# Optimization experiments

Hardware: AMD Instinct MI355X
Metric: run time of the kernel (lower is better)

Reference implementation:

```python
import jax, jax.numpy as jnp
import numpy as np

D_IN = 1024
D_OUT = 1024
NUM_HEAD = 16
HEAD_DIM = D_OUT // NUM_HEAD
CTX = 2048


def setup_inputs() -> dict:
    key = jax.random.key(0)
    ks = jax.random.split(key, 7)
    s = 0.02
    x = jax.random.normal(ks[0], (2, CTX, D_IN), dtype=jnp.float32)
    Wq = jax.random.normal(ks[1], (D_IN, D_OUT), dtype=jnp.float32) * s
    Wk = jax.random.normal(ks[2], (D_IN, D_OUT), dtype=jnp.float32) * s
    Wv = jax.random.normal(ks[3], (D_IN, D_OUT), dtype=jnp.float32) * s
    Wo = jax.random.normal(ks[4], (D_OUT, D_OUT), dtype=jnp.float32) * s
    bo = jax.random.normal(ks[5], (D_OUT,), dtype=jnp.float32) * s
    return {"x": x, "Wq": Wq, "Wk": Wk, "Wv": Wv, "Wo": Wo, "bo": bo}


def reference(x, Wq, Wk, Wv, Wo, bo):
    B, T, _ = x.shape
    # QKV projections, split into heads: [B, H, T, hd]
    def split_heads(y):
        return y.reshape(B, T, NUM_HEAD, HEAD_DIM).transpose(0, 2, 1, 3)
    q = split_heads(x @ Wq)
    k = split_heads(x @ Wk)
    v = split_heads(x @ Wv)
    # scaled causal attention scores [B, H, T, T]
    scores = jnp.einsum("bhqd,bhkd->bhqk", q, k) / jnp.sqrt(
        jnp.asarray(HEAD_DIM, dtype=x.dtype))
    causal = jnp.tril(jnp.ones((T, T), dtype=bool))  # mask buffer triu(diag=1) -> keep lower tri
    scores = jnp.where(causal[None, None], scores, jnp.asarray(-jnp.inf, dtype=x.dtype))
    attn = jax.nn.softmax(scores, axis=-1)
    # dropout with droprate=0.0 is identity
    ctx = jnp.einsum("bhqk,bhkd->bhqd", attn, v)
    ctx = ctx.transpose(0, 2, 1, 3).reshape(B, T, D_OUT)
    return ctx @ Wo + bo
```

## Files before the change

### kernel.cpp

```cpp
#include <hip/hip_runtime.h>

typedef __bf16 bf16x8 __attribute__((ext_vector_type(8)));
typedef float f32x4 __attribute__((ext_vector_type(4)));

__device__ inline float bf2f(unsigned short u) {
    unsigned int x = ((unsigned int)u) << 16;
    return __builtin_bit_cast(float, x);
}
__device__ inline unsigned short f2bf(float f) {
    unsigned int x = __builtin_bit_cast(unsigned int, f);
    x += 0x7fff + ((x >> 16) & 1);
    return (unsigned short)(x >> 16);
}

__device__ __forceinline__ void gl_lds16(const unsigned short* g, unsigned short* l)
{
    __builtin_amdgcn_global_load_lds(
        (const __attribute__((address_space(1))) void*)g,
        (__attribute__((address_space(3))) void*)l, 16, 0, 0);
}

__global__ __launch_bounds__(256)
void prep(const float* __restrict__ x, unsigned short* __restrict__ xb,
          const float* __restrict__ Wq, const float* __restrict__ Wk,
          const float* __restrict__ Wv, unsigned short* __restrict__ wT)
{
    __shared__ unsigned short T[64][72];
    if (blockIdx.x < 2048) {
        const size_t i = ((size_t)blockIdx.x * 256 + threadIdx.x) * 8;
        float4 a = *reinterpret_cast<const float4*>(x + i);
        float4 b = *reinterpret_cast<const float4*>(x + i + 4);
        unsigned short t[8] = { f2bf(a.x), f2bf(a.y), f2bf(a.z), f2bf(a.w),
                                f2bf(b.x), f2bf(b.y), f2bf(b.z), f2bf(b.w) };
        *reinterpret_cast<uint4*>(xb + i) = *reinterpret_cast<uint4*>(t);
        return;
    }
    const int blk = blockIdx.x - 2048;
    const int z = blk >> 8, within = blk & 255;
    const float* W = (z == 0) ? Wq : (z == 1) ? Wk : Wv;
    unsigned short* dstBase = wT + (size_t)z * 1024 * 1024;
    const int k0 = (within >> 4) * 64, n0 = (within & 15) * 64;
    const int r = threadIdx.x >> 2, c0 = (threadIdx.x & 3) * 16;
    const float* src = W + (size_t)(k0 + r) * 1024 + n0 + c0;
    #pragma unroll
    for (int j = 0; j < 16; j += 4) {
        float4 f = *reinterpret_cast<const float4*>(src + j);
        T[r][c0 + j]     = f2bf(f.x);
        T[r][c0 + j + 1] = f2bf(f.y);
        T[r][c0 + j + 2] = f2bf(f.z);
        T[r][c0 + j + 3] = f2bf(f.w);
    }
    __syncthreads();
    unsigned short* dst = dstBase + (size_t)(n0 + r) * 1024 + k0 + c0;
    #pragma unroll
    for (int h = 0; h < 2; ++h) {
        unsigned short t8[8];
        #pragma unroll
        for (int j = 0; j < 8; ++j) t8[j] = T[c0 + h * 8 + j][r];
        *reinterpret_cast<uint4*>(dst + h * 8) = *reinterpret_cast<uint4*>(t8);
    }
}

__global__ __launch_bounds__(256)
void wconv(const float* __restrict__ W, unsigned short* __restrict__ wT)
{
    __shared__ unsigned short T[64][72];
    const int k0 = blockIdx.y * 64, n0 = blockIdx.x * 64;
    const int r = threadIdx.x >> 2, c0 = (threadIdx.x & 3) * 16;
    const float* src = W + (size_t)(k0 + r) * 1024 + n0 + c0;
    #pragma unroll
    for (int j = 0; j < 16; j += 4) {
        float4 f = *reinterpret_cast<const float4*>(src + j);
        T[r][c0 + j]     = f2bf(f.x);
        T[r][c0 + j + 1] = f2bf(f.y);
        T[r][c0 + j + 2] = f2bf(f.z);
        T[r][c0 + j + 3] = f2bf(f.w);
    }
    __syncthreads();
    unsigned short* dst = wT + (size_t)(n0 + r) * 1024 + k0 + c0;
    #pragma unroll
    for (int h = 0; h < 2; ++h) {
        unsigned short t8[8];
        #pragma unroll
        for (int j = 0; j < 8; ++j) t8[j] = T[c0 + h * 8 + j][r];
        *reinterpret_cast<uint4*>(dst + h * 8) = *reinterpret_cast<uint4*>(t8);
    }
}

template <int MODE>
__global__ __launch_bounds__(256)
void gemm128(const unsigned short* __restrict__ A,
             const unsigned short* __restrict__ BT,
             void* __restrict__ C0, void* __restrict__ C1,
             void* __restrict__ C2, const float* __restrict__ bias)
{
    __shared__ unsigned short As[128 * 32];
    __shared__ unsigned short Bs[128 * 32];

    const int tid = threadIdx.x;
    const int wave = tid >> 6, lane = tid & 63, quad = lane >> 4, l16 = lane & 15;
    const int wm = wave >> 1, wn = wave & 1;
    const int mBase = blockIdx.y * 128, nBase = blockIdx.x * 128;

    f32x4 acc[4][4] = {};

    const int srow = lane >> 2, sko = (lane & 3) * 8;

    for (int kb = 0; kb < 1024; kb += 32) {
        __syncthreads();
        #pragma unroll
        for (int j = 0; j < 2; ++j) {
            const int seg = wave * 2 + j;
            gl_lds16(A  + (size_t)(mBase + seg * 16 + srow) * 1024 + kb + sko,
                     As + seg * 512);
            gl_lds16(BT + (size_t)(nBase + seg * 16 + srow) * 1024 + kb + sko,
                     Bs + seg * 512);
        }
        __syncthreads();

        bf16x8 af[4], bf[4];
        #pragma unroll
        for (int t = 0; t < 4; ++t) {
            af[t] = *reinterpret_cast<const bf16x8*>(&As[(wm * 64 + t * 16 + l16) * 32 + quad * 8]);
            bf[t] = *reinterpret_cast<const bf16x8*>(&Bs[(wn * 64 + t * 16 + l16) * 32 + quad * 8]);
        }
        #pragma unroll
        for (int ti = 0; ti < 4; ++ti)
            #pragma unroll
            for (int tj = 0; tj < 4; ++tj)
                acc[ti][tj] = __builtin_amdgcn_mfma_f32_16x16x32_bf16(
                    af[ti], bf[tj], acc[ti][tj], 0, 0, 0);
    }

    #pragma unroll
    for (int ti = 0; ti < 4; ++ti) {
        const int row0 = mBase + wm * 64 + ti * 16 + quad * 4;
        #pragma unroll
        for (int tj = 0; tj < 4; ++tj) {
            const int col = nBase + wn * 64 + tj * 16 + l16;
            if constexpr (MODE == 0) {
                if (col < 1024) {
                    unsigned short* qb = (unsigned short*)C0;
                    #pragma unroll
                    for (int i = 0; i < 4; ++i)
                        qb[(size_t)(row0 + i) * 1024 + col] = f2bf(acc[ti][tj][i]);
                } else if (col < 2048) {
                    unsigned short* kb = (unsigned short*)C1;
                    #pragma unroll
                    for (int i = 0; i < 4; ++i)
                        kb[(size_t)(row0 + i) * 1024 + col - 1024] = f2bf(acc[ti][tj][i]);
                } else {
                    unsigned short* vT = (unsigned short*)C2;
                    unsigned short t4[4] = { f2bf(acc[ti][tj][0]), f2bf(acc[ti][tj][1]),
                                             f2bf(acc[ti][tj][2]), f2bf(acc[ti][tj][3]) };
                    *reinterpret_cast<uint2*>(&vT[(size_t)(col - 2048) * 4096 + row0]) =
                        *reinterpret_cast<uint2*>(t4);
                }
            } else {
                float* out = (float*)C0;
                const float ba = bias[col];
                #pragma unroll
                for (int i = 0; i < 4; ++i)
                    out[(size_t)(row0 + i) * 1024 + col] = acc[ti][tj][i] + ba;
            }
        }
    }
}

#define LDP 72

__global__ __launch_bounds__(256)
void attn6(const unsigned short* __restrict__ q,
           const unsigned short* __restrict__ k,
           const unsigned short* __restrict__ vT,
           unsigned short* __restrict__ ctx)
{
    __shared__ unsigned short Ks[2][2][64 * 32];
    __shared__ unsigned short Vs[2][2][64 * 32];
    __shared__ unsigned short PsA[64 * LDP];
    __shared__ unsigned short PsB[64 * LDP];

    const int tid  = threadIdx.x;
    const int wave = tid >> 6, lane = tid & 63, quad = lane >> 4, l16 = lane & 15;
    const int j  = blockIdx.x;
    const int bh = blockIdx.y;
    const int b = bh >> 4, h = bh & 15;
    const int tokBase = b * 2048;
    const int colBase = h * 64;
    const int qtA = 31 - j, qtB = j;
    const int qBaseA = qtA * 64, qBaseB = qtB * 64;

    bf16x8 aqA[2], aqB[2];
    {
        const unsigned short* qrA =
            q + (size_t)(tokBase + qBaseA + wave * 16 + l16) * 1024 + colBase;
        aqA[0] = *reinterpret_cast<const bf16x8*>(qrA + quad * 8);
        aqA[1] = *reinterpret_cast<const bf16x8*>(qrA + 32 + quad * 8);
        const unsigned short* qrB =
            q + (size_t)(tokBase + qBaseB + wave * 16 + l16) * 1024 + colBase;
        aqB[0] = *reinterpret_cast<const bf16x8*>(qrB + quad * 8);
        aqB[1] = *reinterpret_cast<const bf16x8*>(qrB + 32 + quad * 8);
    }

    f32x4 oA[4] = {}, oB[4] = {};
    float lsA[4] = {}, lsB[4] = {};

    const int sa = lane >> 2;
    const int sb = (lane & 3) * 8;

    auto stage = [&](int tok0, int buf) {
        #pragma unroll
        for (int o = 0; o < 2; ++o) {
            const int op = wave * 2 + o;
            const int hh = op >> 2, rg = op & 3;
            gl_lds16(k + (size_t)(tok0 + rg * 16 + sa) * 1024 + colBase + hh * 32 + sb,
                     &Ks[buf][hh][rg * 16 * 32]);
            gl_lds16(vT + (size_t)(colBase + rg * 16 + sa) * 4096 + tok0 + hh * 32 + sb,
                     &Vs[buf][hh][rg * 16 * 32]);
        }
    };

    stage(tokBase, 0);
    __syncthreads();

    const int nkt = qtA + 1;
    for (int kt = 0; kt < nkt; ++kt) {
        const int buf = kt & 1;
        if (kt + 1 < nkt)
            stage(tokBase + (kt + 1) * 64, buf ^ 1);

        const bool doB = (kt <= qtB);
        const bool diagA = (kt == qtA), diagB = (kt == qtB);

        {
            f32x4 sc[4] = {};
            #pragma unroll
            for (int t = 0; t < 4; ++t)
                #pragma unroll
                for (int kf = 0; kf < 2; ++kf) {
                    bf16x8 bk = *reinterpret_cast<const bf16x8*>(
                        &Ks[buf][kf][(t * 16 + l16) * 32 + quad * 8]);
                    sc[t] = __builtin_amdgcn_mfma_f32_16x16x32_bf16(aqA[kf], bk, sc[t], 0, 0, 0);
                }
            #pragma unroll
            for (int t = 0; t < 4; ++t) {
                const int ki = kt * 64 + t * 16 + l16;
                #pragma unroll
                for (int r = 0; r < 4; ++r) {
                    float p = __expf(sc[t][r] * 0.125f);
                    if (diagA && ki > qBaseA + wave * 16 + quad * 4 + r) p = 0.0f;
                    lsA[r] += p;
                    PsA[(wave * 16 + quad * 4 + r) * LDP + t * 16 + l16] = f2bf(p);
                }
            }
        }
        if (doB) {
            f32x4 sc[4] = {};
            #pragma unroll
            for (int t = 0; t < 4; ++t)
                #pragma unroll
                for (int kf = 0; kf < 2; ++kf) {
                    bf16x8 bk = *reinterpret_cast<const bf16x8*>(
                        &Ks[buf][kf][(t * 16 + l16) * 32 + quad * 8]);
                    sc[t] = __builtin_amdgcn_mfma_f32_16x16x32_bf16(aqB[kf], bk, sc[t], 0, 0, 0);
                }
            #pragma unroll
            for (int t = 0; t < 4; ++t) {
                const int ki = kt * 64 + t * 16 + l16;
                #pragma unroll
                for (int r = 0; r < 4; ++r) {
                    float p = __expf(sc[t][r] * 0.125f);
                    if (diagB && ki > qBaseB + wave * 16 + quad * 4 + r) p = 0.0f;
                    lsB[r] += p;
                    PsB[(wave * 16 + quad * 4 + r) * LDP + t * 16 + l16] = f2bf(p);
                }
            }
        }

        #pragma unroll
        for (int kf = 0; kf < 2; ++kf) {
            if (diagA && (wave * 16 + 15) < kf * 32) continue;
            bf16x8 ap = *reinterpret_cast<const bf16x8*>(
                &PsA[(wave * 16 + l16) * LDP + kf * 32 + quad * 8]);
            #pragma unroll
            for (int t = 0; t < 4; ++t) {
                bf16x8 bv = *reinterpret_cast<const bf16x8*>(
                    &Vs[buf][kf][(t * 16 + l16) * 32 + quad * 8]);
                oA[t] = __builtin_amdgcn_mfma_f32_16x16x32_bf16(ap, bv, oA[t], 0, 0, 0);
            }
        }
        if (doB) {
            #pragma unroll
            for (int kf = 0; kf < 2; ++kf) {
                if (diagB && (wave * 16 + 15) < kf * 32) continue;
                bf16x8 ap = *reinterpret_cast<const bf16x8*>(
                    &PsB[(wave * 16 + l16) * LDP + kf * 32 + quad * 8]);
                #pragma unroll
                for (int t = 0; t < 4; ++t) {
                    bf16x8 bv = *reinterpret_cast<const bf16x8*>(
                        &Vs[buf][kf][(t * 16 + l16) * 32 + quad * 8]);
                    oB[t] = __builtin_amdgcn_mfma_f32_16x16x32_bf16(ap, bv, oB[t], 0, 0, 0);
                }
            }
        }

        if (kt + 1 < nkt)
            __syncthreads();
    }

    #pragma unroll
    for (int off = 1; off < 16; off <<= 1)
        #pragma unroll
        for (int r = 0; r < 4; ++r) {
            lsA[r] += __shfl_xor(lsA[r], off);
            lsB[r] += __shfl_xor(lsB[r], off);
        }

    #pragma unroll
    for (int r = 0; r < 4; ++r) {
        const float invA = 1.0f / lsA[r];
        const float invB = 1.0f / lsB[r];
        const size_t grA = (size_t)(tokBase + qBaseA + wave * 16 + quad * 4 + r) * 1024 + colBase;
        const size_t grB = (size_t)(tokBase + qBaseB + wave * 16 + quad * 4 + r) * 1024 + colBase;
        #pragma unroll
        for (int t = 0; t < 4; ++t) {
            ctx[grA + t * 16 + l16] = f2bf(oA[t][r] * invA);
            ctx[grB + t * 16 + l16] = f2bf(oB[t][r] * invB);
        }
    }
}

extern "C" void kernel_launch(void* const* d_in, const int* in_sizes, int n_in,
                              void* d_out, int out_size, void* d_ws, size_t ws_size,
                              hipStream_t stream)
{
    const float* x  = (const float*)d_in[0];
    const float* Wq = (const float*)d_in[1];
    const float* Wk = (const float*)d_in[2];
    const float* Wv = (const float*)d_in[3];
    const float* Wo = (const float*)d_in[4];
    const float* bo = (const float*)d_in[5];
    float* out = (float*)d_out;

    unsigned short* xb     = (unsigned short*)d_ws;
    unsigned short* qb     = xb + (size_t)4096 * 1024;
    unsigned short* kb     = qb + (size_t)4096 * 1024;
    unsigned short* vT     = kb + (size_t)4096 * 1024;
    unsigned short* ctx    = xb;
    unsigned short* wqkvT  = (unsigned short*)d_out;
    unsigned short* woT    = kb;

    prep<<<2816, 256, 0, stream>>>(x, xb, Wq, Wk, Wv, wqkvT);

    gemm128<0><<<dim3(24, 32), 256, 0, stream>>>(xb, wqkvT, qb, kb, vT, nullptr);

    attn6<<<dim3(16, 32), 256, 0, stream>>>(qb, kb, vT, ctx);

    wconv<<<dim3(16, 16), 256, 0, stream>>>(Wo, woT);

    gemm128<2><<<dim3(8, 32), 256, 0, stream>>>(ctx, woT, out, nullptr, nullptr, bo);
}
```

Measured before the change: 194.2 us.

## Rework attention kernel to 32x32 MFMA with register-resident P and split-K waves

Replaces the 16x16x32 MFMA attention with 32x32x16 MFMA tiles in which each wave handles a 32-query slice and half of each 64-key tile. P stays in registers, packed with v_cvt_pk_bf16 and rearranged with permlane32_swap, instead of round-tripping through LDS. K and V staging uses an XOR-swizzled 64-wide LDS layout to avoid bank conflicts, and the two key halves are reduced through LDS at the end. The goal is fewer LDS writes and reads and larger MFMA instructions, at the cost of more registers (launch bounds of 2) and an extra cross-wave reduction step.

```diff
diff --git a/kernel.cpp b/kernel.cpp
--- a/kernel.cpp
+++ b/kernel.cpp
@@ -2,6 +2,8 @@
 
 typedef __bf16 bf16x8 __attribute__((ext_vector_type(8)));
 typedef float f32x4 __attribute__((ext_vector_type(4)));
+typedef float f32x16 __attribute__((ext_vector_type(16)));
+typedef unsigned int u32x4 __attribute__((ext_vector_type(4)));
 
 __device__ inline float bf2f(unsigned short u) {
     unsigned int x = ((unsigned int)u) << 16;
@@ -167,167 +169,177 @@
     }
 }
 
-#define LDP 72
-
-__global__ __launch_bounds__(256)
-void attn6(const unsigned short* __restrict__ q,
+__global__ __launch_bounds__(256, 2)
+void attn7(const unsigned short* __restrict__ q,
            const unsigned short* __restrict__ k,
            const unsigned short* __restrict__ vT,
            unsigned short* __restrict__ ctx)
 {
-    __shared__ unsigned short Ks[2][2][64 * 32];
-    __shared__ unsigned short Vs[2][2][64 * 32];
-    __shared__ unsigned short PsA[64 * LDP];
-    __shared__ unsigned short PsB[64 * LDP];
+    __shared__ unsigned short Ks[2][64 * 64];
+    __shared__ unsigned short Vs[2][64 * 64];
+    __shared__ float Lt[8 * 64];
 
     const int tid  = threadIdx.x;
-    const int wave = tid >> 6, lane = tid & 63, quad = lane >> 4, l16 = lane & 15;
+    const int wave = tid >> 6, lane = tid & 63;
+    const int q32 = lane & 31, hi = lane >> 5;
+    const int slice = wave & 1;
+    const int ks    = wave >> 1;
     const int j  = blockIdx.x;
     const int bh = blockIdx.y;
     const int b = bh >> 4, h = bh & 15;
     const int tokBase = b * 2048;
     const int colBase = h * 64;
     const int qtA = 31 - j, qtB = j;
-    const int qBaseA = qtA * 64, qBaseB = qtB * 64;
-
-    bf16x8 aqA[2], aqB[2];
+    const int qloA = qtA * 64 + slice * 32;
+    const int qloB = qtB * 64 + slice * 32;
+
+    bf16x8 aqA[4], aqB[4];
     {
-        const unsigned short* qrA =
-            q + (size_t)(tokBase + qBaseA + wave * 16 + l16) * 1024 + colBase;
-        aqA[0] = *reinterpret_cast<const bf16x8*>(qrA + quad * 8);
-        aqA[1] = *reinterpret_cast<const bf16x8*>(qrA + 32 + quad * 8);
-        const unsigned short* qrB =
-            q + (size_t)(tokBase + qBaseB + wave * 16 + l16) * 1024 + colBase;
-        aqB[0] = *reinterpret_cast<const bf16x8*>(qrB + quad * 8);
-        aqB[1] = *reinterpret_cast<const bf16x8*>(qrB + 32 + quad * 8);
-    }
-
-    f32x4 oA[4] = {}, oB[4] = {};
-    float lsA[4] = {}, lsB[4] = {};
-
-    const int sa = lane >> 2;
-    const int sb = (lane & 3) * 8;
+        const unsigned short* ra = q + (size_t)(tokBase + qloA + q32) * 1024 + colBase + hi * 8;
+        const unsigned short* rb = q + (size_t)(tokBase + qloB + q32) * 1024 + colBase + hi * 8;
+        #pragma unroll
+        for (int c = 0; c < 4; ++c) {
+            aqA[c] = *reinterpret_cast<const bf16x8*>(ra + c * 16);
+            aqB[c] = *reinterpret_cast<const bf16x8*>(rb + c * 16);
+        }
+    }
+
+    f32x16 oA[2] = {}, oB[2] = {};
+    float lsA = 0.0f, lsB = 0.0f;
+
+    const int s0 = (wave * 2 + 0) * 64 + lane;
+    const int s1 = (wave * 2 + 1) * 64 + lane;
+    const int r0 = s0 >> 3, sw0 = (s0 & 7) ^ (r0 & 7);
+    const int r1 = s1 >> 3, sw1 = (s1 & 7) ^ (r1 & 7);
+    const size_t kOff0 = (size_t)r0 * 1024 + colBase + sw0 * 8;
+    const size_t kOff1 = (size_t)r1 * 1024 + colBase + sw1 * 8;
+    const size_t vOff0 = (size_t)(colBase + r0) * 4096 + sw0 * 8;
+    const size_t vOff1 = (size_t)(colBase + r1) * 4096 + sw1 * 8;
 
     auto stage = [&](int tok0, int buf) {
-        #pragma unroll
-        for (int o = 0; o < 2; ++o) {
-            const int op = wave * 2 + o;
-            const int hh = op >> 2, rg = op & 3;
-            gl_lds16(k + (size_t)(tok0 + rg * 16 + sa) * 1024 + colBase + hh * 32 + sb,
-                     &Ks[buf][hh][rg * 16 * 32]);
-            gl_lds16(vT + (size_t)(colBase + rg * 16 + sa) * 4096 + tok0 + hh * 32 + sb,
-                     &Vs[buf][hh][rg * 16 * 32]);
-        }
+        gl_lds16(k  + (size_t)tok0 * 1024 + kOff0, &Ks[buf][(wave * 2 + 0) * 512]);
+        gl_lds16(k  + (size_t)tok0 * 1024 + kOff1, &Ks[buf][(wave * 2 + 1) * 512]);
+        gl_lds16(vT + vOff0 + tok0,                &Vs[buf][(wave * 2 + 0) * 512]);
+        gl_lds16(vT + vOff1 + tok0,                &Vs[buf][(wave * 2 + 1) * 512]);
     };
 
+    bf16x8 ak[4];
+    bf16x8 bv[2][2];
+
+    auto tile = [&](const bf16x8 (&aq)[4], f32x16 (&o)[2], float& ls,
+                    int qlo, int klo) {
+        if (klo > qlo + 31) return;
+        f32x16 sc = (f32x16)0.0f;
+        #pragma unroll
+        for (int c = 0; c < 4; ++c)
+            sc = __builtin_amdgcn_mfma_f32_32x32x16_bf16(ak[c], aq[c], sc, 0, 0, 0);
+        float p[16];
+        #pragma unroll
+        for (int r = 0; r < 16; ++r) p[r] = __expf(sc[r] * 0.125f);
+        if (klo + 31 > qlo) {
+            #pragma unroll
+            for (int r = 0; r < 16; ++r) {
+                const int krow = (r & 3) + 8 * (r >> 2) + 4 * hi;
+                if (klo + krow > qlo + q32) p[r] = 0.0f;
+            }
+        }
+        #pragma unroll
+        for (int r = 0; r < 16; ++r) ls += p[r];
+        unsigned int pk[8];
+        #pragma unroll
+        for (int i = 0; i < 8; ++i)
+            asm("v_cvt_pk_bf16_f32 %0, %1, %2"
+                : "=v"(pk[i]) : "v"(p[2 * i]), "v"(p[2 * i + 1]));
+        #pragma unroll
+        for (int kc = 0; kc < 2; ++kc) {
+            unsigned int x0 = pk[kc * 4 + 0], y0 = pk[kc * 4 + 2];
+            unsigned int x1 = pk[kc * 4 + 1], y1 = pk[kc * 4 + 3];
+            asm("v_permlane32_swap_b32 %0, %1" : "+v"(x0), "+v"(y0));
+            asm("v_permlane32_swap_b32 %0, %1" : "+v"(x1), "+v"(y1));
+            const u32x4 wv = { x0, x1, y0, y1 };
+            const bf16x8 pa = __builtin_bit_cast(bf16x8, wv);
+            #pragma unroll
+            for (int dh = 0; dh < 2; ++dh)
+                o[dh] = __builtin_amdgcn_mfma_f32_32x32x16_bf16(pa, bv[kc][dh], o[dh], 0, 0, 0);
+        }
+    };
+
     stage(tokBase, 0);
     __syncthreads();
 
     const int nkt = qtA + 1;
+    int buf = 0;
+    const int krowK = ks * 32 + q32;
     for (int kt = 0; kt < nkt; ++kt) {
-        const int buf = kt & 1;
         if (kt + 1 < nkt)
             stage(tokBase + (kt + 1) * 64, buf ^ 1);
-
-        const bool doB = (kt <= qtB);
-        const bool diagA = (kt == qtA), diagB = (kt == qtB);
-
-        {
-            f32x4 sc[4] = {};
-            #pragma unroll
-            for (int t = 0; t < 4; ++t)
-                #pragma unroll
-                for (int kf = 0; kf < 2; ++kf) {
-                    bf16x8 bk = *reinterpret_cast<const bf16x8*>(
-                        &Ks[buf][kf][(t * 16 + l16) * 32 + quad * 8]);
-                    sc[t] = __builtin_amdgcn_mfma_f32_16x16x32_bf16(aqA[kf], bk, sc[t], 0, 0, 0);
-                }
-            #pragma unroll
-            for (int t = 0; t < 4; ++t) {
-                const int ki = kt * 64 + t * 16 + l16;
-                #pragma unroll
-                for (int r = 0; r < 4; ++r) {
-                    float p = __expf(sc[t][r] * 0.125f);
-                    if (diagA && ki > qBaseA + wave * 16 + quad * 4 + r) p = 0.0f;
-                    lsA[r] += p;
-                    PsA[(wave * 16 + quad * 4 + r) * LDP + t * 16 + l16] = f2bf(p);
-                }
+        const unsigned short* KsB = Ks[buf];
+        const unsigned short* VsB = Vs[buf];
+        #pragma unroll
+        for (int c = 0; c < 4; ++c) {
+            const int u = c * 2 + hi;
+            ak[c] = *reinterpret_cast<const bf16x8*>(
+                &KsB[krowK * 64 + ((u ^ (krowK & 7)) * 8)]);
+        }
+        #pragma unroll
+        for (int kc = 0; kc < 2; ++kc)
+            #pragma unroll
+            for (int dh = 0; dh < 2; ++dh) {
+                const int vrow = dh * 32 + q32;
+                const int u = ks * 4 + kc * 2 + hi;
+                bv[kc][dh] = *reinterpret_cast<const bf16x8*>(
+                    &VsB[vrow * 64 + ((u ^ (vrow & 7)) * 8)]);
             }
-        }
-        if (doB) {
-            f32x4 sc[4] = {};
-            #pragma unroll
-            for (int t = 0; t < 4; ++t)
-                #pragma unroll
-                for (int kf = 0; kf < 2; ++kf) {
-                    bf16x8 bk = *reinterpret_cast<const bf16x8*>(
-                        &Ks[buf][kf][(t * 16 + l16) * 32 + quad * 8]);
-                    sc[t] = __builtin_amdgcn_mfma_f32_16x16x32_bf16(aqB[kf], bk, sc[t], 0, 0, 0);
-                }
-            #pragma unroll
-            for (int t = 0; t < 4; ++t) {
-                const int ki = kt * 64 + t * 16 + l16;
-                #pragma unroll
-                for (int r = 0; r < 4; ++r) {
-                    float p = __expf(sc[t][r] * 0.125f);
-                    if (diagB && ki > qBaseB + wave * 16 + quad * 4 + r) p = 0.0f;
-                    lsB[r] += p;
-                    PsB[(wave * 16 + quad * 4 + r) * LDP + t * 16 + l16] = f2bf(p);
-                }
-            }
-        }
-
-        #pragma unroll
-        for (int kf = 0; kf < 2; ++kf) {
-            if (diagA && (wave * 16 + 15) < kf * 32) continue;
-            bf16x8 ap = *reinterpret_cast<const bf16x8*>(
-                &PsA[(wave * 16 + l16) * LDP + kf * 32 + quad * 8]);
-            #pragma unroll
-            for (int t = 0; t < 4; ++t) {
-                bf16x8 bv = *reinterpret_cast<const bf16x8*>(
-                    &Vs[buf][kf][(t * 16 + l16) * 32 + quad * 8]);
-                oA[t] = __builtin_amdgcn_mfma_f32_16x16x32_bf16(ap, bv, oA[t], 0, 0, 0);
-            }
-        }
-        if (doB) {
-            #pragma unroll
-            for (int kf = 0; kf < 2; ++kf) {
-                if (diagB && (wave * 16 + 15) < kf * 32) continue;
-                bf16x8 ap = *reinterpret_cast<const bf16x8*>(
-                    &PsB[(wave * 16 + l16) * LDP + kf * 32 + quad * 8]);
-                #pragma unroll
-                for (int t = 0; t < 4; ++t) {
-                    bf16x8 bv = *reinterpret_cast<const bf16x8*>(
-                        &Vs[buf][kf][(t * 16 + l16) * 32 + quad * 8]);
-                    oB[t] = __builtin_amdgcn_mfma_f32_16x16x32_bf16(ap, bv, oB[t], 0, 0, 0);
-                }
-            }
-        }
-
+        const int klo = kt * 64 + ks * 32;
+        tile(aqA, oA, lsA, qloA, klo);
+        tile(aqB, oB, lsB, qloB, klo);
         if (kt + 1 < nkt)
             __syncthreads();
-    }
-
-    #pragma unroll
-    for (int off = 1; off < 16; off <<= 1)
-        #pragma unroll
-        for (int r = 0; r < 4; ++r) {
-            lsA[r] += __shfl_xor(lsA[r], off);
-            lsB[r] += __shfl_xor(lsB[r], off);
-        }
-
-    #pragma unroll
-    for (int r = 0; r < 4; ++r) {
-        const float invA = 1.0f / lsA[r];
-        const float invB = 1.0f / lsB[r];
-        const size_t grA = (size_t)(tokBase + qBaseA + wave * 16 + quad * 4 + r) * 1024 + colBase;
-        const size_t grB = (size_t)(tokBase + qBaseB + wave * 16 + quad * 4 + r) * 1024 + colBase;
-        #pragma unroll
-        for (int t = 0; t < 4; ++t) {
-            ctx[grA + t * 16 + l16] = f2bf(oA[t][r] * invA);
-            ctx[grB + t * 16 + l16] = f2bf(oB[t][r] * invB);
-        }
-    }
+        buf ^= 1;
+    }
+
+    float* Obuf = reinterpret_cast<float*>(&Ks[0][0]);
+
+    __syncthreads();
+    Lt[(wave * 2 + 0) * 64 + lane] = lsA;
+    Lt[(wave * 2 + 1) * 64 + lane] = lsB;
+
+    auto writePartial = [&](const f32x16 (&o)[2]) {
+        float* slot = Obuf + slice * 2048;
+        #pragma unroll
+        for (int r = 0; r < 16; ++r) {
+            const int row = (r & 3) + 8 * (r >> 2) + 4 * hi;
+            #pragma unroll
+            for (int dh = 0; dh < 2; ++dh)
+                slot[row * 64 + dh * 32 + q32] = o[dh][r];
+        }
+    };
+    auto finalize = [&](int t, int qt, const f32x16 (&o)[2]) {
+        const float lf = Lt[(slice * 2 + t) * 64 + q32]
+                       + Lt[(slice * 2 + t) * 64 + 32 + q32]
+                       + Lt[((slice + 2) * 2 + t) * 64 + q32]
+                       + Lt[((slice + 2) * 2 + t) * 64 + 32 + q32];
+        const float inv = 1.0f / lf;
+        const float* slot = Obuf + slice * 2048;
+        #pragma unroll
+        for (int r = 0; r < 16; ++r) {
+            const int row = (r & 3) + 8 * (r >> 2) + 4 * hi;
+            const float invr = __shfl(inv, row);
+            const size_t gr = (size_t)(tokBase + qt * 64 + slice * 32 + row) * 1024 + colBase;
+            #pragma unroll
+            for (int dh = 0; dh < 2; ++dh)
+                ctx[gr + dh * 32 + q32] =
+                    f2bf((o[dh][r] + slot[row * 64 + dh * 32 + q32]) * invr);
+        }
+    };
+
+    if (ks == 1) writePartial(oA);
+    __syncthreads();
+    if (ks == 0) finalize(0, qtA, oA);
+    __syncthreads();
+    if (ks == 0) writePartial(oB);
+    __syncthreads();
+    if (ks == 1) finalize(1, qtB, oB);
 }
 
 extern "C" void kernel_launch(void* const* d_in, const int* in_sizes, int n_in,
@@ -354,7 +366,7 @@
 
     gemm128<0><<<dim3(24, 32), 256, 0, stream>>>(xb, wqkvT, qb, kb, vT, nullptr);
 
-    attn6<<<dim3(16, 32), 256, 0, stream>>>(qb, kb, vT, ctx);
+    attn7<<<dim3(16, 32), 256, 0, stream>>>(qb, kb, vT, ctx);
 
     wconv<<<dim3(16, 16), 256, 0, stream>>>(Wo, woT);
 
```

After: 183.3 us. 1.06x faster.
